# Performance work log

Measured on AMD Instinct MI355X. Metric: run time of the kernel, lower is better.

Reference implementation:

```python
import jax, jax.numpy as jnp
import numpy as np
import math

N_ATOMS = 128
BATCH = 8
FEAT = 64
K_BASIS = 16
N_IRR = 9            # (max_degree+1)^2 with max_degree=2
CUTOFF = 5.0
N_ELEM = 119
SQ3 = 1.7320508075688772

# degree of each of the 9 irrep components: l = 0,1,1,1,2,2,2,2,2
DEG = np.array([0, 1, 1, 1, 2, 2, 2, 2, 2])
_BINOM = jnp.asarray([math.comb(K_BASIS - 1, k) for k in range(K_BASIS)], dtype=jnp.float32)
_KPOW = jnp.arange(K_BASIS, dtype=jnp.float32)


def _sph(u):
    # real spherical harmonics up to l=2 of unit vectors u: [E,3] -> [E,9]
    ux, uy, uz = u[:, 0], u[:, 1], u[:, 2]
    return jnp.stack([
        jnp.ones_like(ux),
        ux, uy, uz,
        SQ3 * ux * uy, SQ3 * uy * uz, 0.5 * (3.0 * uz * uz - 1.0),
        SQ3 * ux * uz, 0.5 * SQ3 * (ux * ux - uy * uy),
    ], axis=-1)


def _basis(disp):
    # disp: [E,3] -> basis [E, 9, K]: Y_lm(u) * reciprocal-Bernstein radial * smooth cutoff
    r = jnp.sqrt(jnp.sum(disp * disp, axis=-1) + 1e-12)      # [E]
    Y = _sph(disp / r[:, None])                              # [E,9]
    w = 1.0 / (1.0 + r)                                      # reciprocal mapping to (0,1]
    rad = _BINOM * w[:, None] ** _KPOW * (1.0 - w)[:, None] ** (K_BASIS - 1.0 - _KPOW)  # [E,K]
    t = (r / CUTOFF) ** 2
    cut = jnp.where(t < 1.0, jnp.exp(1.0 - 1.0 / jnp.maximum(1.0 - t, 1e-12)), 0.0)     # [E]
    return Y[:, :, None] * (rad * cut[:, None])[:, None, :]


def _energy_single(z, pos, embed, WA, WB, W1, b1, W2, W1s, b1s, W2s, w_out, element_bias, dst, src):
    n = pos.shape[0]
    disp = pos[src] - pos[dst]                               # [E,3]
    B = _basis(disp)                                         # [E,9,K]
    # embed atomic numbers into the scalar (l=0) channel
    x = jnp.zeros((n, N_IRR, FEAT), pos.dtype).at[:, 0, :].set(embed[z])
    for i in range(2):  # full-degree message-passing iterations
        xs = x[src]                                          # gather  [E,9,F]
        # equivariant product paths: (scalar src) x (tensor basis) and (tensor src) x (scalar basis)
        mA = jnp.einsum('elk,kf,ef->elf', B, WA[i], xs[:, 0, :])
        mB = xs * jnp.einsum('ek,kf->ef', B[:, 0, :], WB[i])[:, None, :]
        y = jax.ops.segment_sum(mA + mB, dst, num_segments=n)  # scatter-add [N,9,F]
        y = x + y
        y = jnp.einsum('nlf,lfg->nlg', y, W1[i][DEG]).at[:, 0, :].add(b1[i])  # per-degree Dense
        s = y[:, 0, :]
        y = jnp.concatenate([jax.nn.silu(s)[:, None, :],
                             y[:, 1:, :] * jax.nn.sigmoid(s)[:, None, :]], axis=1)  # gated silu
        y = jnp.einsum('nlf,lfg->nlg', y, W2[i][DEG])
        x = x + y
    # last iteration: degree-0 output only (invariant contraction of all degrees)
    xs = x[src]
    mA = jnp.einsum('ek,kf,ef->ef', B[:, 0, :], WA[2], xs[:, 0, :])
    mB = jnp.einsum('elk,elf,kf->ef', B, xs, WB[2])
    y = jax.ops.segment_sum(mA + mB, dst, num_segments=n)    # [N,F]
    x0 = x[:, 0, :]
    h = x0 + y
    h = jax.nn.silu(h @ W1s + b1s) @ W2s
    x0 = x0 + h
    atomic_energies = x0 @ w_out + element_bias[z]           # [N]
    return jnp.sum(atomic_energies)


def setup_inputs() -> dict:
    ks = jax.random.split(jax.random.key(0), 16)
    ii, jj = np.meshgrid(np.arange(N_ATOMS), np.arange(N_ATOMS), indexing='ij')
    mask = ii != jj
    s = 1.0 / np.sqrt(FEAT)
    return {
        'features': jax.random.randint(ks[0], (BATCH, N_ATOMS), 1, N_ELEM, dtype=jnp.int32),
        'positions': jax.random.uniform(ks[1], (BATCH, N_ATOMS, 3), jnp.float32) * 12.0,
        'embed': 0.5 * jax.random.normal(ks[2], (N_ELEM, FEAT), jnp.float32),
        'WA': 0.1 * jax.random.normal(ks[3], (3, K_BASIS, FEAT), jnp.float32),
        'WB': 0.1 * jax.random.normal(ks[4], (3, K_BASIS, FEAT), jnp.float32),
        'W1': s * jax.random.normal(ks[5], (2, 3, FEAT, FEAT), jnp.float32),
        'b1': jnp.zeros((2, FEAT), jnp.float32),
        'W2': 0.1 * s * jax.random.normal(ks[6], (2, 3, FEAT, FEAT), jnp.float32),
        'W1s': s * jax.random.normal(ks[7], (FEAT, FEAT), jnp.float32),
        'b1s': jnp.zeros((FEAT,), jnp.float32),
        'W2s': 0.1 * s * jax.random.normal(ks[8], (FEAT, FEAT), jnp.float32),
        'w_out': 0.1 * jax.random.normal(ks[9], (FEAT,), jnp.float32),
        'element_bias': 0.01 * jax.random.normal(ks[10], (N_ELEM,), jnp.float32),
        'dst_idx': jnp.asarray(ii[mask], jnp.int32),
        'src_idx': jnp.asarray(jj[mask], jnp.int32),
    }


def reference(features, positions, embed, WA, WB, W1, b1, W2, W1s, b1s, W2s, w_out, element_bias, dst_idx, src_idx):
    params = (embed, WA, WB, W1, b1, W2, W1s, b1s, W2s, w_out, element_bias)

    def per_sample(z, pos):
        E, g = jax.value_and_grad(
            lambda p: _energy_single(z, p, *params, dst_idx, src_idx))(pos)
        return E, -g  # energy, forces = -dE/dpos

    return jax.vmap(per_sample)(features, positions)
```

## Files before the change

kernel.cpp:

```cpp
#include <hip/hip_runtime.h>
#include <math.h>

namespace {

constexpr int F   = 64;
constexpr int NA  = 128;
constexpr int NB  = 8;
constexpr int EPN = NA*(NA-1);
constexpr int K   = 16;
constexpr int L   = 9;
constexpr int BE  = NB*EPN;
constexpr int NNLF= NB*NA*L*F;
constexpr int BNF = NB*NA*F;
constexpr int GSP = 8;
constexpr int NSUB= 16;
constexpr float SQ3 = 1.7320508075688772f;

typedef float v2f __attribute__((ext_vector_type(2)));

__device__ __constant__ float BINOM[16] = {1.f,15.f,105.f,455.f,1365.f,3003.f,5005.f,6435.f,
                                           6435.f,5005.f,3003.f,1365.f,455.f,105.f,15.f,1.f};
__device__ __constant__ int DEGC[9] = {0,1,1,1,2,2,2,2,2};

__device__ inline float wred(float v){
  #pragma unroll
  for (int o=32;o>0;o>>=1) v += __shfl_xor(v, o, 64);
  return v;
}

__device__ inline float qreduce(float v0, float v1, float v2, float v3, int lane){
  float a = ((lane&1)? v1 : v0) + __shfl_xor(((lane&1)? v0 : v1), 1, 64);
  float b = ((lane&1)? v3 : v2) + __shfl_xor(((lane&1)? v2 : v3), 1, 64);
  float r = ((lane&2)? b : a) + __shfl_xor(((lane&2)? a : b), 2, 64);
  r += __shfl_xor(r, 4, 64);
  r += __shfl_xor(r, 8, 64);
  r += __shfl_xor(r,16, 64);
  r += __shfl_xor(r,32, 64);
  return r;
}

__global__ void k_prep(const float* W1, const float* W2, const float* W1s,
                       const float* W2s, const float* wout,
                       float* W1T, float* W2T, float* W1sT, float* dsp,
                       float* outbuf){
  int idx = blockIdx.x*256 + threadIdx.x;
  if (idx < 6*F*F){
    int rem = idx % (F*F); int m = idx/(F*F); int g = rem/F, f = rem%F;
    W1T[idx] = W1[(m*F+f)*F+g];
    W2T[idx] = W2[(m*F+f)*F+g];
  } else if (idx < 6*F*F + F*F){
    int rem = idx - 6*F*F; int g = rem/F, f = rem%F;
    W1sT[rem] = W1s[f*F+g];
  } else if (idx < 6*F*F + F*F + F){
    int f = idx - 6*F*F - F*F;
    float s=0.f;
    for (int g=0; g<F; g++) s += W2s[f*F+g]*wout[g];
    dsp[f]=s;
  } else if (idx < 6*F*F + F*F + F + NB + NB*NA*3){
    outbuf[idx - (6*F*F + F*F + F)] = 0.f;
  }
}

__global__ void k_geom(const float* __restrict__ pos, const int* __restrict__ dsti,
                       const int* __restrict__ srci,
                       float* __restrict__ U, float* __restrict__ Rr,
                       float* __restrict__ Rp){
  int idx = blockIdx.x*256 + threadIdx.x;
  if (idx >= BE) return;
  int b = idx / EPN, e = idx % EPN;
  int d = dsti[e], s = srci[e];
  const float* pb = pos + (size_t)b*NA*3;
  float dx = pb[s*3+0]-pb[d*3+0];
  float dy = pb[s*3+1]-pb[d*3+1];
  float dz = pb[s*3+2]-pb[d*3+2];
  float ss = dx*dx+dy*dy+dz*dz + 1e-12f;
  float r  = sqrtf(ss);
  float ir = 1.f/r;
  U[(size_t)idx*4+0]=dx*ir; U[(size_t)idx*4+1]=dy*ir;
  U[(size_t)idx*4+2]=dz*ir; U[(size_t)idx*4+3]=ir;
  float w = 1.f/(1.f+r), v = 1.f - w;
  float wp[16], vp[16];
  wp[0]=1.f; vp[0]=1.f;
  #pragma unroll
  for (int k=1;k<16;k++){ wp[k]=wp[k-1]*w; vp[k]=vp[k-1]*v; }
  float t = (r*0.2f)*(r*0.2f);
  float cut=0.f, dcut=0.f;
  if (t < 1.f){
    float e1 = 1.f - t;
    float m  = fmaxf(e1, 1e-12f);
    cut = expf(1.f - 1.f/m);
    if (e1 > 1e-12f) dcut = -cut/(e1*e1) * (2.f*r*0.04f);
  }
  float nww = -w*w;
  #pragma unroll
  for (int k=0;k<16;k++){
    float rad = BINOM[k]*wp[k]*vp[15-k];
    float t1 = (k>0)  ? (float)k      * wp[k-1]*vp[15-k] : 0.f;
    float t2 = (k<15) ? (float)(15-k) * wp[k]  *vp[14-k] : 0.f;
    float dradr = BINOM[k]*(t1-t2)*nww;
    Rr[(size_t)idx*16+k] = rad*cut;
    Rp[(size_t)idx*16+k] = dradr*cut + rad*dcut;
  }
}

__global__ void k_init_x(const int* __restrict__ z, const float* __restrict__ embed,
                         float* __restrict__ x0){
  int b = blockIdx.x / NA, n = blockIdx.x % NA, f = threadIdx.x;
  int zi = z[b*NA+n];
  float* row = x0 + ((size_t)(b*NA+n))*L*F;
  row[f] = embed[(size_t)zi*F+f];
  #pragma unroll
  for (int l=1;l<L;l++) row[l*F+f]=0.f;
}

template<bool FIRST>
__global__ __launch_bounds__(64,6) void k_edge_fwd(const float* __restrict__ x,
    const float* __restrict__ WA, const float* __restrict__ WB,
    const float* __restrict__ U, const float* __restrict__ Rr,
    float* __restrict__ aggP){
  int bid = blockIdx.x;
  int g = bid & (GSP-1), bn = bid >> 3;
  int b = bn >> 7, n = bn & (NA-1);
  int f = threadIdx.x;
  v2f wab[K];
  #pragma unroll
  for (int k=0;k<K;k++){ v2f t = {WA[k*F+f], WB[k*F+f]}; wab[k]=t; }
  float acc[L];
  #pragma unroll
  for (int l=0;l<L;l++) acc[l]=0.f;
  const float* xb = x + (size_t)b*NA*L*F;
  int c0 = g*NSUB, c1 = min(c0+NSUB, NA-1);
  #pragma unroll 2
  for (int c=c0; c<c1; ++c){
    int e = n*(NA-1)+c;
    int j = c + (c>=n);
    size_t ge = (size_t)b*EPN + e;
    const float* Re = Rr + ge*K;
    v2f AB = {0.f, 0.f};
    #pragma unroll
    for (int k=0;k<K;k++) AB += Re[k]*wab[k];
    float RA=AB.x, RB=AB.y;
    float ux=U[ge*4+0], uy=U[ge*4+1], uz=U[ge*4+2];
    float Y4=SQ3*ux*uy, Y5=SQ3*uy*uz, Y6=0.5f*(3.f*uz*uz-1.f);
    float Y7=SQ3*ux*uz, Y8=0.5f*SQ3*(ux*ux-uy*uy);
    const float* xr = xb + (size_t)j*L*F + f;
    float xs0 = xr[0];
    float t1 = RA*xs0;
    acc[0] += t1 + xs0*RB;
    if (FIRST){
      acc[1] += ux*t1; acc[2] += uy*t1; acc[3] += uz*t1;
      acc[4] += Y4*t1; acc[5] += Y5*t1; acc[6] += Y6*t1;
      acc[7] += Y7*t1; acc[8] += Y8*t1;
    } else {
      acc[1] += ux*t1 + xr[1*F]*RB;
      acc[2] += uy*t1 + xr[2*F]*RB;
      acc[3] += uz*t1 + xr[3*F]*RB;
      acc[4] += Y4*t1 + xr[4*F]*RB;
      acc[5] += Y5*t1 + xr[5*F]*RB;
      acc[6] += Y6*t1 + xr[6*F]*RB;
      acc[7] += Y7*t1 + xr[7*F]*RB;
      acc[8] += Y8*t1 + xr[8*F]*RB;
    }
  }
  float* ar = aggP + (size_t)g*NNLF + (size_t)bn*L*F + f;
  #pragma unroll
  for (int l=0;l<L;l++) ar[l*F] = acc[l];
}

__global__ __launch_bounds__(256) void k_node_fwd(const float* __restrict__ x,
    const float* __restrict__ aggP, const float* __restrict__ W1,
    const float* __restrict__ b1, const float* __restrict__ W2,
    float* __restrict__ y2out, float* __restrict__ xout){
  __shared__ float sh[L*F];
  __shared__ float yb[L*F];
  __shared__ float zb[L*F];
  int t = threadIdx.x, g = t&63, w = t>>6;
  size_t base = ((size_t)blockIdx.x)*L*F;
  for (int idx=t; idx<L*F; idx+=256){
    float s = x[base+idx];
    #pragma unroll
    for (int sl=0; sl<GSP; sl++) s += aggP[(size_t)sl*NNLF + base + idx];
    sh[idx]=s;
  }
  __syncthreads();
  for (int l=w; l<L; l+=4){
    const float* W = W1 + DEGC[l]*F*F + g;
    float s=0.f;
    for (int ff=0; ff<F; ff++) s += sh[l*F+ff]*W[(size_t)ff*F];
    if (l==0) s += b1[g];
    y2out[base+l*F+g]=s;
    yb[l*F+g]=s;
  }
  __syncthreads();
  float sv = yb[g];
  float sg = 1.f/(1.f+expf(-sv));
  for (int l=w; l<L; l+=4)
    zb[l*F+g] = (l==0)? sv*sg : yb[l*F+g]*sg;
  __syncthreads();
  for (int l=w; l<L; l+=4){
    const float* W = W2 + DEGC[l]*F*F + g;
    float s=0.f;
    for (int ff=0; ff<F; ff++) s += zb[l*F+ff]*W[(size_t)ff*F];
    xout[base+l*F+g] = x[base+l*F+g] + s;
  }
}

__global__ __launch_bounds__(64,6) void k_redge_fwd(const float* __restrict__ x2,
    const float* __restrict__ WA2, const float* __restrict__ WB2,
    const float* __restrict__ U, const float* __restrict__ Rr,
    float* __restrict__ yRp){
  int bid = blockIdx.x;
  int g = bid & (GSP-1), bn = bid >> 3;
  int b = bn >> 7, n = bn & (NA-1);
  int f = threadIdx.x;
  v2f wab[K];
  #pragma unroll
  for (int k=0;k<K;k++){ v2f t = {WA2[k*F+f], WB2[k*F+f]}; wab[k]=t; }
  float acc=0.f;
  const float* xb = x2 + (size_t)b*NA*L*F;
  int c0 = g*NSUB, c1 = min(c0+NSUB, NA-1);
  #pragma unroll 2
  for (int c=c0; c<c1; ++c){
    int e = n*(NA-1)+c;
    int j = c + (c>=n);
    size_t ge = (size_t)b*EPN + e;
    const float* Re = Rr + ge*K;
    v2f AB = {0.f, 0.f};
    #pragma unroll
    for (int k=0;k<K;k++) AB += Re[k]*wab[k];
    float RA=AB.x, RB=AB.y;
    float ux=U[ge*4+0], uy=U[ge*4+1], uz=U[ge*4+2];
    const float* xr = xb + (size_t)j*L*F + f;
    float xs0 = xr[0];
    float T = xs0
            + ux*xr[1*F] + uy*xr[2*F] + uz*xr[3*F]
            + (SQ3*ux*uy)*xr[4*F] + (SQ3*uy*uz)*xr[5*F]
            + (0.5f*(3.f*uz*uz-1.f))*xr[6*F]
            + (SQ3*ux*uz)*xr[7*F] + (0.5f*SQ3*(ux*ux-uy*uy))*xr[8*F];
    acc += RA*xs0 + RB*T;
  }
  yRp[(size_t)g*BNF + (size_t)bn*F + f] = acc;
}

__global__ __launch_bounds__(256) void k_rnode_fwd(const int* __restrict__ z,
    const float* __restrict__ x2, const float* __restrict__ yRp,
    const float* __restrict__ W1s, const float* __restrict__ b1s,
    const float* __restrict__ W2s, const float* __restrict__ wout,
    const float* __restrict__ ebias, float* __restrict__ pW, float* Eout){
  __shared__ float sh[F];
  __shared__ float part[4][F];
  int t = threadIdx.x, g = t&63, w = t>>6;
  int bnn = blockIdx.x;
  int b = bnn >> 7;
  size_t base = (size_t)bnn*L*F;
  size_t nb   = (size_t)bnn*F;
  if (t < F){
    float s = x2[base+t];
    #pragma unroll
    for (int sl=0; sl<GSP; sl++) s += yRp[(size_t)sl*BNF + nb + t];
    sh[t]=s;
  }
  __syncthreads();
  float pp=0.f;
  for (int ff=w*16; ff<w*16+16; ff++) pp += sh[ff]*W1s[(size_t)ff*F+g];
  part[w][g]=pp;
  __syncthreads();
  float p = part[0][g]+part[1][g]+part[2][g]+part[3][g] + b1s[g];
  if (w==0) pW[nb+g]=p;
  float sp = p/(1.f+expf(-p));
  __syncthreads();
  if (w==0) sh[g]=sp;
  __syncthreads();
  float h=0.f;
  for (int ff=w*16; ff<w*16+16; ff++) h += sh[ff]*W2s[(size_t)ff*F+g];
  part[w][g]=h;
  __syncthreads();
  if (w==0){
    float h2 = part[0][g]+part[1][g]+part[2][g]+part[3][g];
    float x0v = x2[base+g];
    float en = wred((x0v+h2)*wout[g]);
    if (g==0) atomicAdd(Eout+b, en + ebias[z[bnn]]);
  }
}

__global__ __launch_bounds__(256) void k_rnode_bwd(const float* __restrict__ pW,
    const float* __restrict__ dsp, const float* __restrict__ W1sT,
    const float* __restrict__ wout, float* __restrict__ dyR, float* __restrict__ dxA){
  __shared__ float sh[F];
  __shared__ float part[4][F];
  int t = threadIdx.x, g = t&63, w = t>>6;
  size_t nb = (size_t)blockIdx.x*F;
  size_t base = (size_t)blockIdx.x*L*F;
  if (t < F){
    float p  = pW[nb+t];
    float sgm = 1.f/(1.f+expf(-p));
    sh[t] = dsp[t]*sgm*(1.f + p*(1.f-sgm));
  }
  __syncthreads();
  float s=0.f;
  for (int ff=w*16; ff<w*16+16; ff++) s += sh[ff]*W1sT[(size_t)ff*F+g];
  part[w][g]=s;
  __syncthreads();
  if (w==0){
    float dh1 = part[0][g]+part[1][g]+part[2][g]+part[3][g];
    dyR[nb+g]=dh1;
    dxA[base+g] = wout[g]+dh1;
  }
  for (int idx=t; idx<(L-1)*F; idx+=256) dxA[base+F+idx]=0.f;
}

__global__ __launch_bounds__(64,6) void k_redge_bwd(const float* __restrict__ x2,
    const float* __restrict__ WA2, const float* __restrict__ WB2,
    const float* __restrict__ U, const float* __restrict__ Rr,
    const float* __restrict__ Rp, const float* __restrict__ dyR,
    float* __restrict__ partP, float* Fout){
  int bid = blockIdx.x;
  int g = bid & (GSP-1), bn = bid >> 3;
  int b = bn >> 7, j = bn & (NA-1);
  int f = threadIdx.x, m = f & 3;
  v2f wab[K];
  #pragma unroll
  for (int k=0;k<K;k++){ v2f t = {WA2[k*F+f], WB2[k*F+f]}; wab[k]=t; }
  size_t xbase = ((size_t)bn)*L*F;
  float xs[L];
  #pragma unroll
  for (int l=0;l<L;l++) xs[l]=x2[xbase+l*F+f];
  float acc[L];
  #pragma unroll
  for (int l=0;l<L;l++) acc[l]=0.f;
  float sdd=0.f;
  int i0 = g*NSUB, i1 = min(i0+NSUB, NA-1);
  #pragma unroll 2
  for (int ii=i0; ii<i1; ++ii){
    int i = ii + (ii>=j);
    int c = (j<i)? j : j-1;
    size_t ge = (size_t)b*EPN + i*(NA-1)+c;
    float gv = dyR[(size_t)(b*NA+i)*F+f];
    const float* Re = Rr + ge*K;
    const float* Pe = Rp + ge*K;
    v2f RAB = {0.f,0.f}, PAB = {0.f,0.f};
    #pragma unroll
    for (int k=0;k<K;k++){ RAB += Re[k]*wab[k]; PAB += Pe[k]*wab[k]; }
    float RA=RAB.x, RB=RAB.y, PA=PAB.x, PB=PAB.y;
    float ux=U[ge*4+0], uy=U[ge*4+1], uz=U[ge*4+2], ir=U[ge*4+3];
    float Y4=SQ3*ux*uy, Y5=SQ3*uy*uz, Y6=0.5f*(3.f*uz*uz-1.f);
    float Y7=SQ3*ux*uz, Y8=0.5f*SQ3*(ux*ux-uy*uy);
    float T = xs[0] + ux*xs[1]+uy*xs[2]+uz*xs[3]
            + Y4*xs[4]+Y5*xs[5]+Y6*xs[6]+Y7*xs[7]+Y8*xs[8];
    float X0 = xs[1] + SQ3*(uy*xs[4]+uz*xs[7]+ux*xs[8]);
    float X1 = xs[2] + SQ3*(ux*xs[4]+uz*xs[5]-uy*xs[8]);
    float X2 = xs[3] + SQ3*(uy*xs[5]+ux*xs[7]) + 3.f*uz*xs[6];
    acc[0] += gv*(RA+RB);
    acc[1] += gv*ux*RB; acc[2] += gv*uy*RB; acc[3] += gv*uz*RB;
    acc[4] += gv*Y4*RB; acc[5] += gv*Y5*RB; acc[6] += gv*Y6*RB;
    acc[7] += gv*Y7*RB; acc[8] += gv*Y8*RB;
    float gRB = gv*RB;
    float r4 = qreduce(gRB*X0, gRB*X1, gRB*X2, gv*(xs[0]*PA + T*PB), f);
    float um = (m==0)?ux : (m==1)?uy : (m==2)?uz : 0.f;
    float q = r4*um;
    q += __shfl_xor(q,1,64); q += __shfl_xor(q,2,64);
    float SR = __shfl(r4, f|3, 64);
    float dd = (r4 - q*um)*ir + SR*um;
    if (f<3) atomicAdd(&Fout[(size_t)(b*NA+i)*3+f], dd);
    sdd += dd;
  }
  float* ar = partP + (size_t)g*NNLF + xbase + f;
  #pragma unroll
  for (int l=0;l<L;l++) ar[l*F] = acc[l];
  if (f<3) atomicAdd(&Fout[(size_t)(b*NA+j)*3+f], -sdd);
}

template<bool WDX>
__global__ __launch_bounds__(256) void k_node_bwd(const float* __restrict__ dxIn,
    const float* __restrict__ partP, const float* __restrict__ y2W,
    const float* __restrict__ W1T, const float* __restrict__ W2T,
    float* __restrict__ dagg, float* __restrict__ dxOut){
  __shared__ float A[L*F];
  __shared__ float D3[L*F];
  __shared__ float Bb[L*F];
  __shared__ float prt[4][F];
  int t = threadIdx.x, g = t&63, w = t>>6;
  size_t base = ((size_t)blockIdx.x)*L*F;
  for (int idx=t; idx<L*F; idx+=256){
    float s = dxIn[base+idx];
    #pragma unroll
    for (int sl=0; sl<GSP; sl++) s += partP[(size_t)sl*NNLF + base + idx];
    A[idx]=s;
  }
  __syncthreads();
  float pc=0.f;
  for (int l=w; l<L; l+=4){
    const float* W = W2T + DEGC[l]*F*F + g;
    float s=0.f;
    for (int ff=0; ff<F; ff++) s += A[l*F+ff]*W[(size_t)ff*F];
    D3[l*F+g]=s;
    if (l>0) pc += s * y2W[base+l*F+g];
  }
  prt[w][g]=pc;
  __syncthreads();
  float sv = y2W[base+g];
  float sg = 1.f/(1.f+expf(-sv));
  for (int l=w; l<L; l+=4){
    float v;
    if (l==0){
      float sum = prt[0][g]+prt[1][g]+prt[2][g]+prt[3][g];
      v = D3[g]*sg*(1.f+sv*(1.f-sg)) + sum*sg*(1.f-sg);
    } else {
      v = D3[l*F+g]*sg;
    }
    Bb[l*F+g]=v;
  }
  __syncthreads();
  for (int l=w; l<L; l+=4){
    const float* W = W1T + DEGC[l]*F*F + g;
    float s=0.f;
    for (int ff=0; ff<F; ff++) s += Bb[l*F+ff]*W[(size_t)ff*F];
    dagg[base+l*F+g]=s;
    if (WDX) dxOut[base+l*F+g] = A[l*F+g] + s;
  }
}

template<bool WDX, bool FIRST>
__global__ __launch_bounds__(64,6) void k_edge_bwd(const float* __restrict__ xI,
    const float* __restrict__ WA, const float* __restrict__ WB,
    const float* __restrict__ U, const float* __restrict__ Rr,
    const float* __restrict__ Rp, const float* __restrict__ dagg,
    float* __restrict__ partP, float* Fout){
  int bid = blockIdx.x;
  int g = bid & (GSP-1), bn = bid >> 3;
  int b = bn >> 7, j = bn & (NA-1);
  int f = threadIdx.x, m = f & 3;
  v2f wab[K];
  #pragma unroll
  for (int k=0;k<K;k++){ v2f t = {WA[k*F+f], WB[k*F+f]}; wab[k]=t; }
  size_t xbase = ((size_t)bn)*L*F;
  float xs[L];
  xs[0] = xI[xbase+f];
  #pragma unroll
  for (int l=1;l<L;l++) xs[l] = FIRST ? 0.f : xI[xbase+l*F+f];
  float acc[L]; float acc0=0.f;
  #pragma unroll
  for (int l=0;l<L;l++) acc[l]=0.f;
  float sdd=0.f;
  int i0 = g*NSUB, i1 = min(i0+NSUB, NA-1);
  #pragma unroll 2
  for (int ii=i0; ii<i1; ++ii){
    int i = ii + (ii>=j);
    int c = (j<i)? j : j-1;
    size_t ge = (size_t)b*EPN + i*(NA-1)+c;
    const float* gr = dagg + ((size_t)(b*NA+i))*L*F + f;
    float gl[L];
    #pragma unroll
    for (int l=0;l<L;l++) gl[l]=gr[l*F];
    const float* Re = Rr + ge*K;
    const float* Pe = Rp + ge*K;
    v2f RAB = {0.f,0.f}, PAB = {0.f,0.f};
    #pragma unroll
    for (int k=0;k<K;k++){ RAB += Re[k]*wab[k]; PAB += Pe[k]*wab[k]; }
    float RA=RAB.x, RB=RAB.y, PA=PAB.x, PB=PAB.y;
    float ux=U[ge*4+0], uy=U[ge*4+1], uz=U[ge*4+2], ir=U[ge*4+3];
    float Y4=SQ3*ux*uy, Y5=SQ3*uy*uz, Y6=0.5f*(3.f*uz*uz-1.f);
    float Y7=SQ3*ux*uz, Y8=0.5f*SQ3*(ux*ux-uy*uy);
    float gy = gl[0] + gl[1]*ux+gl[2]*uy+gl[3]*uz
             + gl[4]*Y4+gl[5]*Y5+gl[6]*Y6+gl[7]*Y7+gl[8]*Y8;
    float gx;
    if (FIRST){
      gx = gl[0]*xs[0];
    } else {
      gx = 0.f;
      #pragma unroll
      for (int l=0;l<L;l++) gx += gl[l]*xs[l];
    }
    float G0 = gl[1] + SQ3*(uy*gl[4]+uz*gl[7]+ux*gl[8]);
    float G1 = gl[2] + SQ3*(ux*gl[4]+uz*gl[5]-uy*gl[8]);
    float G2 = gl[3] + SQ3*(uy*gl[5]+ux*gl[7]) + 3.f*uz*gl[6];
    if (WDX){
      acc0 += gy*RA;
      #pragma unroll
      for (int l=0;l<L;l++) acc[l] += gl[l]*RB;
    }
    float cm = RA*xs[0];
    float r4 = qreduce(cm*G0, cm*G1, cm*G2, gy*xs[0]*PA + gx*PB, f);
    float um = (m==0)?ux : (m==1)?uy : (m==2)?uz : 0.f;
    float q = r4*um;
    q += __shfl_xor(q,1,64); q += __shfl_xor(q,2,64);
    float SR = __shfl(r4, f|3, 64);
    float dd = (r4 - q*um)*ir + SR*um;
    if (f<3) atomicAdd(&Fout[(size_t)(b*NA+i)*3+f], dd);
    sdd += dd;
  }
  if (WDX){
    float* ar = partP + (size_t)g*NNLF + xbase + f;
    ar[0] = acc0 + acc[0];
    #pragma unroll
    for (int l=1;l<L;l++) ar[l*F] = acc[l];
  }
  if (f<3) atomicAdd(&Fout[(size_t)(b*NA+j)*3+f], -sdd);
}

}

extern "C" void kernel_launch(void* const* d_in, const int* in_sizes, int n_in,
                              void* d_out, int out_size, void* d_ws, size_t ws_size,
                              hipStream_t stream){
  (void)in_sizes; (void)n_in; (void)out_size; (void)ws_size;
  const int*   z     = (const int*)  d_in[0];
  const float* pos   = (const float*)d_in[1];
  const float* emb   = (const float*)d_in[2];
  const float* WA    = (const float*)d_in[3];
  const float* WB    = (const float*)d_in[4];
  const float* W1    = (const float*)d_in[5];
  const float* b1    = (const float*)d_in[6];
  const float* W2    = (const float*)d_in[7];
  const float* W1s   = (const float*)d_in[8];
  const float* b1s   = (const float*)d_in[9];
  const float* W2s   = (const float*)d_in[10];
  const float* wout  = (const float*)d_in[11];
  const float* ebias = (const float*)d_in[12];
  const int*   dsti  = (const int*)  d_in[13];
  const int*   srci  = (const int*)  d_in[14];

  float* w    = (float*)d_ws;
  float* U    = w;
  float* Rr   = U    + (size_t)BE*4;
  float* Rp   = Rr   + (size_t)BE*16;
  float* x0   = Rp   + (size_t)BE*16;
  float* x1   = x0   + NNLF;
  float* x2   = x1   + NNLF;
  float* y2b  = x2   + NNLF;
  float* part = y2b  + 2*(size_t)NNLF;
  float* yRp  = part + (size_t)GSP*NNLF;
  float* pW   = yRp  + (size_t)GSP*BNF;
  float* dyR  = pW   + BNF;
  float* dxA  = dyR  + BNF;
  float* dxO  = dxA  + NNLF;
  float* dagg = dxO  + NNLF;
  float* W1T  = dagg + NNLF;
  float* W2T  = W1T  + 6*F*F;
  float* W1sT = W2T  + 6*F*F;
  float* dspv = W1sT + F*F;

  float* Eout = (float*)d_out;
  float* Fout = Eout + NB;

  dim3 bn(NB*NA);
  dim3 be(NB*NA*GSP);

  k_prep  <<<126, 256, 0, stream>>>(W1, W2, W1s, W2s, wout, W1T, W2T, W1sT, dspv, Eout);
  k_geom  <<<(BE+255)/256, 256, 0, stream>>>(pos, dsti, srci, U, Rr, Rp);
  k_init_x<<<bn, 64, 0, stream>>>(z, emb, x0);

  k_edge_fwd<true ><<<be, 64, 0, stream>>>(x0, WA,     WB,     U, Rr, part);
  k_node_fwd<<<bn, 256, 0, stream>>>(x0, part, W1,       b1,   W2,       y2b,      x1);
  k_edge_fwd<false><<<be, 64, 0, stream>>>(x1, WA+K*F, WB+K*F, U, Rr, part);
  k_node_fwd<<<bn, 256, 0, stream>>>(x1, part, W1+3*F*F, b1+F, W2+3*F*F, y2b+NNLF, x2);
  k_redge_fwd<<<be, 64, 0, stream>>>(x2, WA+2*K*F, WB+2*K*F, U, Rr, yRp);
  k_rnode_fwd<<<bn, 256, 0, stream>>>(z, x2, yRp, W1s, b1s, W2s, wout, ebias, pW, Eout);

  k_rnode_bwd<<<bn, 256, 0, stream>>>(pW, dspv, W1sT, wout, dyR, dxA);
  k_redge_bwd<<<be, 64, 0, stream>>>(x2, WA+2*K*F, WB+2*K*F, U, Rr, Rp, dyR, part, Fout);
  k_node_bwd<true ><<<bn, 256, 0, stream>>>(dxA, part, y2b+NNLF, W1T+3*F*F, W2T+3*F*F, dagg, dxO);
  k_edge_bwd<true ,false><<<be, 64, 0, stream>>>(x1, WA+K*F, WB+K*F, U, Rr, Rp, dagg, part, Fout);
  k_node_bwd<false><<<bn, 256, 0, stream>>>(dxO, part, y2b, W1T, W2T, dagg, nullptr);
  k_edge_bwd<false,true ><<<be, 64, 0, stream>>>(x0, WA, WB, U, Rr, Rp, dagg, nullptr, Fout);
}
```

Before: 421.7 us.

## Reduce edge partials in-block via shared memory instead of global partial buffers

Edge kernels now launch one 512-thread block per node, with eight wavefronts each covering a slice of neighbours. Their partial sums are reduced in LDS and written once (or added into dxA/dxO), so node kernels no longer read eight global partial slabs. Per-node force atomics are also collapsed to one per block, and the tangential projection in the force term is folded algebraically so one shuffle reduction disappears. Larger blocks with a __syncthreads may limit occupancy compared with the many small 64-thread blocks used before.

```diff
diff --git a/kernel.cpp b/kernel.cpp
--- a/kernel.cpp
+++ b/kernel.cpp
@@ -12,7 +12,7 @@
 constexpr int BE  = NB*EPN;
 constexpr int NNLF= NB*NA*L*F;
 constexpr int BNF = NB*NA*F;
-constexpr int GSP = 8;
+constexpr int WPB = 8;
 constexpr int NSUB= 16;
 constexpr float SQ3 = 1.7320508075688772f;
 
@@ -114,22 +114,22 @@
 }
 
 template<bool FIRST>
-__global__ __launch_bounds__(64,6) void k_edge_fwd(const float* __restrict__ x,
+__global__ __launch_bounds__(512,8) void k_edge_fwd(const float* __restrict__ x,
     const float* __restrict__ WA, const float* __restrict__ WB,
     const float* __restrict__ U, const float* __restrict__ Rr,
-    float* __restrict__ aggP){
-  int bid = blockIdx.x;
-  int g = bid & (GSP-1), bn = bid >> 3;
+    float* __restrict__ agg){
+  __shared__ float sh[WPB][L*F];
+  int bn = blockIdx.x;
   int b = bn >> 7, n = bn & (NA-1);
-  int f = threadIdx.x;
+  int t = threadIdx.x, f = t&63, wv = t>>6;
   v2f wab[K];
   #pragma unroll
-  for (int k=0;k<K;k++){ v2f t = {WA[k*F+f], WB[k*F+f]}; wab[k]=t; }
+  for (int k=0;k<K;k++){ v2f tt = {WA[k*F+f], WB[k*F+f]}; wab[k]=tt; }
   float acc[L];
   #pragma unroll
   for (int l=0;l<L;l++) acc[l]=0.f;
   const float* xb = x + (size_t)b*NA*L*F;
-  int c0 = g*NSUB, c1 = min(c0+NSUB, NA-1);
+  int c0 = wv*NSUB, c1 = min(c0+NSUB, NA-1);
   #pragma unroll 2
   for (int c=c0; c<c1; ++c){
     int e = n*(NA-1)+c;
@@ -162,13 +162,20 @@
       acc[8] += Y8*t1 + xr[8*F]*RB;
     }
   }
-  float* ar = aggP + (size_t)g*NNLF + (size_t)bn*L*F + f;
-  #pragma unroll
-  for (int l=0;l<L;l++) ar[l*F] = acc[l];
+  #pragma unroll
+  for (int l=0;l<L;l++) sh[wv][l*F+f] = acc[l];
+  __syncthreads();
+  float* ar = agg + (size_t)bn*L*F;
+  for (int idx=t; idx<L*F; idx+=512){
+    float s = sh[0][idx];
+    #pragma unroll
+    for (int w8=1; w8<WPB; w8++) s += sh[w8][idx];
+    ar[idx] = s;
+  }
 }
 
 __global__ __launch_bounds__(256) void k_node_fwd(const float* __restrict__ x,
-    const float* __restrict__ aggP, const float* __restrict__ W1,
+    const float* __restrict__ agg, const float* __restrict__ W1,
     const float* __restrict__ b1, const float* __restrict__ W2,
     float* __restrict__ y2out, float* __restrict__ xout){
   __shared__ float sh[L*F];
@@ -176,12 +183,8 @@
   __shared__ float zb[L*F];
   int t = threadIdx.x, g = t&63, w = t>>6;
   size_t base = ((size_t)blockIdx.x)*L*F;
-  for (int idx=t; idx<L*F; idx+=256){
-    float s = x[base+idx];
-    #pragma unroll
-    for (int sl=0; sl<GSP; sl++) s += aggP[(size_t)sl*NNLF + base + idx];
-    sh[idx]=s;
-  }
+  for (int idx=t; idx<L*F; idx+=256)
+    sh[idx] = x[base+idx] + agg[base+idx];
   __syncthreads();
   for (int l=w; l<L; l+=4){
     const float* W = W1 + DEGC[l]*F*F + g;
@@ -205,20 +208,20 @@
   }
 }
 
-__global__ __launch_bounds__(64,6) void k_redge_fwd(const float* __restrict__ x2,
+__global__ __launch_bounds__(512,8) void k_redge_fwd(const float* __restrict__ x2,
     const float* __restrict__ WA2, const float* __restrict__ WB2,
     const float* __restrict__ U, const float* __restrict__ Rr,
-    float* __restrict__ yRp){
-  int bid = blockIdx.x;
-  int g = bid & (GSP-1), bn = bid >> 3;
+    float* __restrict__ yR){
+  __shared__ float sh[WPB][F];
+  int bn = blockIdx.x;
   int b = bn >> 7, n = bn & (NA-1);
-  int f = threadIdx.x;
+  int t = threadIdx.x, f = t&63, wv = t>>6;
   v2f wab[K];
   #pragma unroll
-  for (int k=0;k<K;k++){ v2f t = {WA2[k*F+f], WB2[k*F+f]}; wab[k]=t; }
+  for (int k=0;k<K;k++){ v2f tt = {WA2[k*F+f], WB2[k*F+f]}; wab[k]=tt; }
   float acc=0.f;
   const float* xb = x2 + (size_t)b*NA*L*F;
-  int c0 = g*NSUB, c1 = min(c0+NSUB, NA-1);
+  int c0 = wv*NSUB, c1 = min(c0+NSUB, NA-1);
   #pragma unroll 2
   for (int c=c0; c<c1; ++c){
     int e = n*(NA-1)+c;
@@ -239,11 +242,18 @@
             + (SQ3*ux*uz)*xr[7*F] + (0.5f*SQ3*(ux*ux-uy*uy))*xr[8*F];
     acc += RA*xs0 + RB*T;
   }
-  yRp[(size_t)g*BNF + (size_t)bn*F + f] = acc;
+  sh[wv][f]=acc;
+  __syncthreads();
+  if (t < F){
+    float s = sh[0][t];
+    #pragma unroll
+    for (int w8=1; w8<WPB; w8++) s += sh[w8][t];
+    yR[(size_t)bn*F + t] = s;
+  }
 }
 
 __global__ __launch_bounds__(256) void k_rnode_fwd(const int* __restrict__ z,
-    const float* __restrict__ x2, const float* __restrict__ yRp,
+    const float* __restrict__ x2, const float* __restrict__ yR,
     const float* __restrict__ W1s, const float* __restrict__ b1s,
     const float* __restrict__ W2s, const float* __restrict__ wout,
     const float* __restrict__ ebias, float* __restrict__ pW, float* Eout){
@@ -254,12 +264,7 @@
   int b = bnn >> 7;
   size_t base = (size_t)bnn*L*F;
   size_t nb   = (size_t)bnn*F;
-  if (t < F){
-    float s = x2[base+t];
-    #pragma unroll
-    for (int sl=0; sl<GSP; sl++) s += yRp[(size_t)sl*BNF + nb + t];
-    sh[t]=s;
-  }
+  if (t < F) sh[t] = x2[base+t] + yR[nb+t];
   __syncthreads();
   float pp=0.f;
   for (int ff=w*16; ff<w*16+16; ff++) pp += sh[ff]*W1s[(size_t)ff*F+g];
@@ -309,18 +314,19 @@
   for (int idx=t; idx<(L-1)*F; idx+=256) dxA[base+F+idx]=0.f;
 }
 
-__global__ __launch_bounds__(64,6) void k_redge_bwd(const float* __restrict__ x2,
+__global__ __launch_bounds__(512,8) void k_redge_bwd(const float* __restrict__ x2,
     const float* __restrict__ WA2, const float* __restrict__ WB2,
     const float* __restrict__ U, const float* __restrict__ Rr,
     const float* __restrict__ Rp, const float* __restrict__ dyR,
-    float* __restrict__ partP, float* Fout){
-  int bid = blockIdx.x;
-  int g = bid & (GSP-1), bn = bid >> 3;
+    float* __restrict__ dxA, float* Fout){
+  __shared__ float sh[WPB][L*F];
+  __shared__ float shS[WPB][4];
+  int bn = blockIdx.x;
   int b = bn >> 7, j = bn & (NA-1);
-  int f = threadIdx.x, m = f & 3;
+  int t = threadIdx.x, f = t&63, wv = t>>6, m = f&3;
   v2f wab[K];
   #pragma unroll
-  for (int k=0;k<K;k++){ v2f t = {WA2[k*F+f], WB2[k*F+f]}; wab[k]=t; }
+  for (int k=0;k<K;k++){ v2f tt = {WA2[k*F+f], WB2[k*F+f]}; wab[k]=tt; }
   size_t xbase = ((size_t)bn)*L*F;
   float xs[L];
   #pragma unroll
@@ -329,7 +335,7 @@
   #pragma unroll
   for (int l=0;l<L;l++) acc[l]=0.f;
   float sdd=0.f;
-  int i0 = g*NSUB, i1 = min(i0+NSUB, NA-1);
+  int i0 = wv*NSUB, i1 = min(i0+NSUB, NA-1);
   #pragma unroll 2
   for (int ii=i0; ii<i1; ++ii){
     int i = ii + (ii>=j);
@@ -355,24 +361,37 @@
     acc[4] += gv*Y4*RB; acc[5] += gv*Y5*RB; acc[6] += gv*Y6*RB;
     acc[7] += gv*Y7*RB; acc[8] += gv*Y8*RB;
     float gRB = gv*RB;
-    float r4 = qreduce(gRB*X0, gRB*X1, gRB*X2, gv*(xs[0]*PA + T*PB), f);
+    float dotX = ux*X0 + uy*X1 + uz*X2;
+    float v3 = gv*(xs[0]*PA + T*PB) - gRB*dotX*ir;
+    float r4 = qreduce(gRB*X0, gRB*X1, gRB*X2, v3, f);
+    float SR = __shfl(r4, f|3, 64);
     float um = (m==0)?ux : (m==1)?uy : (m==2)?uz : 0.f;
-    float q = r4*um;
-    q += __shfl_xor(q,1,64); q += __shfl_xor(q,2,64);
-    float SR = __shfl(r4, f|3, 64);
-    float dd = (r4 - q*um)*ir + SR*um;
+    float dd = r4*ir + SR*um;
     if (f<3) atomicAdd(&Fout[(size_t)(b*NA+i)*3+f], dd);
     sdd += dd;
   }
-  float* ar = partP + (size_t)g*NNLF + xbase + f;
-  #pragma unroll
-  for (int l=0;l<L;l++) ar[l*F] = acc[l];
-  if (f<3) atomicAdd(&Fout[(size_t)(b*NA+j)*3+f], -sdd);
+  #pragma unroll
+  for (int l=0;l<L;l++) sh[wv][l*F+f]=acc[l];
+  if (f<3) shS[wv][f]=sdd;
+  __syncthreads();
+  float* ar = dxA + xbase;
+  for (int idx=t; idx<L*F; idx+=512){
+    float s = sh[0][idx];
+    #pragma unroll
+    for (int w8=1; w8<WPB; w8++) s += sh[w8][idx];
+    ar[idx] += s;
+  }
+  if (t<3){
+    float s = shS[0][t];
+    #pragma unroll
+    for (int w8=1; w8<WPB; w8++) s += shS[w8][t];
+    atomicAdd(&Fout[(size_t)bn*3+t], -s);
+  }
 }
 
 template<bool WDX>
 __global__ __launch_bounds__(256) void k_node_bwd(const float* __restrict__ dxIn,
-    const float* __restrict__ partP, const float* __restrict__ y2W,
+    const float* __restrict__ y2W,
     const float* __restrict__ W1T, const float* __restrict__ W2T,
     float* __restrict__ dagg, float* __restrict__ dxOut){
   __shared__ float A[L*F];
@@ -381,12 +400,7 @@
   __shared__ float prt[4][F];
   int t = threadIdx.x, g = t&63, w = t>>6;
   size_t base = ((size_t)blockIdx.x)*L*F;
-  for (int idx=t; idx<L*F; idx+=256){
-    float s = dxIn[base+idx];
-    #pragma unroll
-    for (int sl=0; sl<GSP; sl++) s += partP[(size_t)sl*NNLF + base + idx];
-    A[idx]=s;
-  }
+  for (int idx=t; idx<L*F; idx+=256) A[idx]=dxIn[base+idx];
   __syncthreads();
   float pc=0.f;
   for (int l=w; l<L; l+=4){
@@ -421,18 +435,19 @@
 }
 
 template<bool WDX, bool FIRST>
-__global__ __launch_bounds__(64,6) void k_edge_bwd(const float* __restrict__ xI,
+__global__ __launch_bounds__(512,8) void k_edge_bwd(const float* __restrict__ xI,
     const float* __restrict__ WA, const float* __restrict__ WB,
     const float* __restrict__ U, const float* __restrict__ Rr,
     const float* __restrict__ Rp, const float* __restrict__ dagg,
-    float* __restrict__ partP, float* Fout){
-  int bid = blockIdx.x;
-  int g = bid & (GSP-1), bn = bid >> 3;
+    float* __restrict__ dxOut, float* Fout){
+  __shared__ float sh[WPB][L*F];
+  __shared__ float shS[WPB][4];
+  int bn = blockIdx.x;
   int b = bn >> 7, j = bn & (NA-1);
-  int f = threadIdx.x, m = f & 3;
+  int t = threadIdx.x, f = t&63, wv = t>>6, m = f&3;
   v2f wab[K];
   #pragma unroll
-  for (int k=0;k<K;k++){ v2f t = {WA[k*F+f], WB[k*F+f]}; wab[k]=t; }
+  for (int k=0;k<K;k++){ v2f tt = {WA[k*F+f], WB[k*F+f]}; wab[k]=tt; }
   size_t xbase = ((size_t)bn)*L*F;
   float xs[L];
   xs[0] = xI[xbase+f];
@@ -442,7 +457,7 @@
   #pragma unroll
   for (int l=0;l<L;l++) acc[l]=0.f;
   float sdd=0.f;
-  int i0 = g*NSUB, i1 = min(i0+NSUB, NA-1);
+  int i0 = wv*NSUB, i1 = min(i0+NSUB, NA-1);
   #pragma unroll 2
   for (int ii=i0; ii<i1; ++ii){
     int i = ii + (ii>=j);
@@ -480,22 +495,37 @@
       for (int l=0;l<L;l++) acc[l] += gl[l]*RB;
     }
     float cm = RA*xs[0];
-    float r4 = qreduce(cm*G0, cm*G1, cm*G2, gy*xs[0]*PA + gx*PB, f);
+    float dotG = ux*G0 + uy*G1 + uz*G2;
+    float v3 = gy*xs[0]*PA + gx*PB - cm*dotG*ir;
+    float r4 = qreduce(cm*G0, cm*G1, cm*G2, v3, f);
+    float SR = __shfl(r4, f|3, 64);
     float um = (m==0)?ux : (m==1)?uy : (m==2)?uz : 0.f;
-    float q = r4*um;
-    q += __shfl_xor(q,1,64); q += __shfl_xor(q,2,64);
-    float SR = __shfl(r4, f|3, 64);
-    float dd = (r4 - q*um)*ir + SR*um;
+    float dd = r4*ir + SR*um;
     if (f<3) atomicAdd(&Fout[(size_t)(b*NA+i)*3+f], dd);
     sdd += dd;
   }
   if (WDX){
-    float* ar = partP + (size_t)g*NNLF + xbase + f;
-    ar[0] = acc0 + acc[0];
-    #pragma unroll
-    for (int l=1;l<L;l++) ar[l*F] = acc[l];
-  }
-  if (f<3) atomicAdd(&Fout[(size_t)(b*NA+j)*3+f], -sdd);
+    sh[wv][f] = acc0 + acc[0];
+    #pragma unroll
+    for (int l=1;l<L;l++) sh[wv][l*F+f] = acc[l];
+  }
+  if (f<3) shS[wv][f]=sdd;
+  __syncthreads();
+  if (WDX){
+    float* ar = dxOut + xbase;
+    for (int idx=t; idx<L*F; idx+=512){
+      float s = sh[0][idx];
+      #pragma unroll
+      for (int w8=1; w8<WPB; w8++) s += sh[w8][idx];
+      ar[idx] += s;
+    }
+  }
+  if (t<3){
+    float s = shS[0][t];
+    #pragma unroll
+    for (int w8=1; w8<WPB; w8++) s += shS[w8][t];
+    atomicAdd(&Fout[(size_t)bn*3+t], -s);
+  }
 }
 
 }
@@ -528,9 +558,9 @@
   float* x1   = x0   + NNLF;
   float* x2   = x1   + NNLF;
   float* y2b  = x2   + NNLF;
-  float* part = y2b  + 2*(size_t)NNLF;
-  float* yRp  = part + (size_t)GSP*NNLF;
-  float* pW   = yRp  + (size_t)GSP*BNF;
+  float* agg  = y2b  + 2*(size_t)NNLF;
+  float* yR   = agg  + NNLF;
+  float* pW   = yR   + BNF;
   float* dyR  = pW   + BNF;
   float* dxA  = dyR  + BNF;
   float* dxO  = dxA  + NNLF;
@@ -544,23 +574,22 @@
   float* Fout = Eout + NB;
 
   dim3 bn(NB*NA);
-  dim3 be(NB*NA*GSP);
 
   k_prep  <<<126, 256, 0, stream>>>(W1, W2, W1s, W2s, wout, W1T, W2T, W1sT, dspv, Eout);
   k_geom  <<<(BE+255)/256, 256, 0, stream>>>(pos, dsti, srci, U, Rr, Rp);
   k_init_x<<<bn, 64, 0, stream>>>(z, emb, x0);
 
-  k_edge_fwd<true ><<<be, 64, 0, stream>>>(x0, WA,     WB,     U, Rr, part);
-  k_node_fwd<<<bn, 256, 0, stream>>>(x0, part, W1,       b1,   W2,       y2b,      x1);
-  k_edge_fwd<false><<<be, 64, 0, stream>>>(x1, WA+K*F, WB+K*F, U, Rr, part);
-  k_node_fwd<<<bn, 256, 0, stream>>>(x1, part, W1+3*F*F, b1+F, W2+3*F*F, y2b+NNLF, x2);
-  k_redge_fwd<<<be, 64, 0, stream>>>(x2, WA+2*K*F, WB+2*K*F, U, Rr, yRp);
-  k_rnode_fwd<<<bn, 256, 0, stream>>>(z, x2, yRp, W1s, b1s, W2s, wout, ebias, pW, Eout);
+  k_edge_fwd<true ><<<bn, 512, 0, stream>>>(x0, WA,     WB,     U, Rr, agg);
+  k_node_fwd<<<bn, 256, 0, stream>>>(x0, agg, W1,       b1,   W2,       y2b,      x1);
+  k_edge_fwd<false><<<bn, 512, 0, stream>>>(x1, WA+K*F, WB+K*F, U, Rr, agg);
+  k_node_fwd<<<bn, 256, 0, stream>>>(x1, agg, W1+3*F*F, b1+F, W2+3*F*F, y2b+NNLF, x2);
+  k_redge_fwd<<<bn, 512, 0, stream>>>(x2, WA+2*K*F, WB+2*K*F, U, Rr, yR);
+  k_rnode_fwd<<<bn, 256, 0, stream>>>(z, x2, yR, W1s, b1s, W2s, wout, ebias, pW, Eout);
 
   k_rnode_bwd<<<bn, 256, 0, stream>>>(pW, dspv, W1sT, wout, dyR, dxA);
-  k_redge_bwd<<<be, 64, 0, stream>>>(x2, WA+2*K*F, WB+2*K*F, U, Rr, Rp, dyR, part, Fout);
-  k_node_bwd<true ><<<bn, 256, 0, stream>>>(dxA, part, y2b+NNLF, W1T+3*F*F, W2T+3*F*F, dagg, dxO);
-  k_edge_bwd<true ,false><<<be, 64, 0, stream>>>(x1, WA+K*F, WB+K*F, U, Rr, Rp, dagg, part, Fout);
-  k_node_bwd<false><<<bn, 256, 0, stream>>>(dxO, part, y2b, W1T, W2T, dagg, nullptr);
-  k_edge_bwd<false,true ><<<be, 64, 0, stream>>>(x0, WA, WB, U, Rr, Rp, dagg, nullptr, Fout);
-}
+  k_redge_bwd<<<bn, 512, 0, stream>>>(x2, WA+2*K*F, WB+2*K*F, U, Rr, Rp, dyR, dxA, Fout);
+  k_node_bwd<true ><<<bn, 256, 0, stream>>>(dxA, y2b+NNLF, W1T+3*F*F, W2T+3*F*F, dagg, dxO);
+  k_edge_bwd<true ,false><<<bn, 512, 0, stream>>>(x1, WA+K*F, WB+K*F, U, Rr, Rp, dagg, dxO, Fout);
+  k_node_bwd<false><<<bn, 256, 0, stream>>>(dxO, y2b, W1T, W2T, dagg, nullptr);
+  k_edge_bwd<false,true ><<<bn, 512, 0, stream>>>(x0, WA, WB, U, Rr, Rp, dagg, nullptr, Fout);
+}
```

After: 1.042 ms. 147% more time.

## Halve edge-kernel grid split, fold force projection into the reduction, drop packed math

Applied to the files above, without the earlier changes.

The per-node edge range is now split into 4 sub-blocks of 32 edges instead of 8 of 16, and launch bounds drop from 6 to 4 waves. That means fewer partial-sum buffers and weight reloads, but also less parallelism in flight. The packed v2f multiply-adds become scalar dual accumulators, and the unroll-2 pragma is removed from the backward loops. In the backward kernels the radial projection term is folded algebraically into the fourth qreduce lane, which removes two shuffles and a multiply per edge.

```diff
diff --git a/kernel.cpp b/kernel.cpp
--- a/kernel.cpp
+++ b/kernel.cpp
@@ -12,11 +12,9 @@
 constexpr int BE  = NB*EPN;
 constexpr int NNLF= NB*NA*L*F;
 constexpr int BNF = NB*NA*F;
-constexpr int GSP = 8;
-constexpr int NSUB= 16;
+constexpr int GSP = 4;
+constexpr int NSUB= 32;
 constexpr float SQ3 = 1.7320508075688772f;
-
-typedef float v2f __attribute__((ext_vector_type(2)));
 
 __device__ __constant__ float BINOM[16] = {1.f,15.f,105.f,455.f,1365.f,3003.f,5005.f,6435.f,
                                            6435.f,5005.f,3003.f,1365.f,455.f,105.f,15.f,1.f};
@@ -114,17 +112,17 @@
 }
 
 template<bool FIRST>
-__global__ __launch_bounds__(64,6) void k_edge_fwd(const float* __restrict__ x,
+__global__ __launch_bounds__(64,4) void k_edge_fwd(const float* __restrict__ x,
     const float* __restrict__ WA, const float* __restrict__ WB,
     const float* __restrict__ U, const float* __restrict__ Rr,
     float* __restrict__ aggP){
   int bid = blockIdx.x;
-  int g = bid & (GSP-1), bn = bid >> 3;
+  int g = bid & (GSP-1), bn = bid >> 2;
   int b = bn >> 7, n = bn & (NA-1);
   int f = threadIdx.x;
-  v2f wab[K];
-  #pragma unroll
-  for (int k=0;k<K;k++){ v2f t = {WA[k*F+f], WB[k*F+f]}; wab[k]=t; }
+  float wa[K], wb[K];
+  #pragma unroll
+  for (int k=0;k<K;k++){ wa[k]=WA[k*F+f]; wb[k]=WB[k*F+f]; }
   float acc[L];
   #pragma unroll
   for (int l=0;l<L;l++) acc[l]=0.f;
@@ -136,10 +134,9 @@
     int j = c + (c>=n);
     size_t ge = (size_t)b*EPN + e;
     const float* Re = Rr + ge*K;
-    v2f AB = {0.f, 0.f};
-    #pragma unroll
-    for (int k=0;k<K;k++) AB += Re[k]*wab[k];
-    float RA=AB.x, RB=AB.y;
+    float RA=0.f, RB=0.f;
+    #pragma unroll
+    for (int k=0;k<K;k++){ float rk=Re[k]; RA += rk*wa[k]; RB += rk*wb[k]; }
     float ux=U[ge*4+0], uy=U[ge*4+1], uz=U[ge*4+2];
     float Y4=SQ3*ux*uy, Y5=SQ3*uy*uz, Y6=0.5f*(3.f*uz*uz-1.f);
     float Y7=SQ3*ux*uz, Y8=0.5f*SQ3*(ux*ux-uy*uy);
@@ -205,17 +202,17 @@
   }
 }
 
-__global__ __launch_bounds__(64,6) void k_redge_fwd(const float* __restrict__ x2,
+__global__ __launch_bounds__(64,4) void k_redge_fwd(const float* __restrict__ x2,
     const float* __restrict__ WA2, const float* __restrict__ WB2,
     const float* __restrict__ U, const float* __restrict__ Rr,
     float* __restrict__ yRp){
   int bid = blockIdx.x;
-  int g = bid & (GSP-1), bn = bid >> 3;
+  int g = bid & (GSP-1), bn = bid >> 2;
   int b = bn >> 7, n = bn & (NA-1);
   int f = threadIdx.x;
-  v2f wab[K];
-  #pragma unroll
-  for (int k=0;k<K;k++){ v2f t = {WA2[k*F+f], WB2[k*F+f]}; wab[k]=t; }
+  float wa[K], wb[K];
+  #pragma unroll
+  for (int k=0;k<K;k++){ wa[k]=WA2[k*F+f]; wb[k]=WB2[k*F+f]; }
   float acc=0.f;
   const float* xb = x2 + (size_t)b*NA*L*F;
   int c0 = g*NSUB, c1 = min(c0+NSUB, NA-1);
@@ -225,10 +222,9 @@
     int j = c + (c>=n);
     size_t ge = (size_t)b*EPN + e;
     const float* Re = Rr + ge*K;
-    v2f AB = {0.f, 0.f};
-    #pragma unroll
-    for (int k=0;k<K;k++) AB += Re[k]*wab[k];
-    float RA=AB.x, RB=AB.y;
+    float RA=0.f, RB=0.f;
+    #pragma unroll
+    for (int k=0;k<K;k++){ float rk=Re[k]; RA += rk*wa[k]; RB += rk*wb[k]; }
     float ux=U[ge*4+0], uy=U[ge*4+1], uz=U[ge*4+2];
     const float* xr = xb + (size_t)j*L*F + f;
     float xs0 = xr[0];
@@ -309,18 +305,18 @@
   for (int idx=t; idx<(L-1)*F; idx+=256) dxA[base+F+idx]=0.f;
 }
 
-__global__ __launch_bounds__(64,6) void k_redge_bwd(const float* __restrict__ x2,
+__global__ __launch_bounds__(64,4) void k_redge_bwd(const float* __restrict__ x2,
     const float* __restrict__ WA2, const float* __restrict__ WB2,
     const float* __restrict__ U, const float* __restrict__ Rr,
     const float* __restrict__ Rp, const float* __restrict__ dyR,
     float* __restrict__ partP, float* Fout){
   int bid = blockIdx.x;
-  int g = bid & (GSP-1), bn = bid >> 3;
+  int g = bid & (GSP-1), bn = bid >> 2;
   int b = bn >> 7, j = bn & (NA-1);
   int f = threadIdx.x, m = f & 3;
-  v2f wab[K];
-  #pragma unroll
-  for (int k=0;k<K;k++){ v2f t = {WA2[k*F+f], WB2[k*F+f]}; wab[k]=t; }
+  float wa[K], wb[K];
+  #pragma unroll
+  for (int k=0;k<K;k++){ wa[k]=WA2[k*F+f]; wb[k]=WB2[k*F+f]; }
   size_t xbase = ((size_t)bn)*L*F;
   float xs[L];
   #pragma unroll
@@ -330,7 +326,6 @@
   for (int l=0;l<L;l++) acc[l]=0.f;
   float sdd=0.f;
   int i0 = g*NSUB, i1 = min(i0+NSUB, NA-1);
-  #pragma unroll 2
   for (int ii=i0; ii<i1; ++ii){
     int i = ii + (ii>=j);
     int c = (j<i)? j : j-1;
@@ -338,10 +333,10 @@
     float gv = dyR[(size_t)(b*NA+i)*F+f];
     const float* Re = Rr + ge*K;
     const float* Pe = Rp + ge*K;
-    v2f RAB = {0.f,0.f}, PAB = {0.f,0.f};
-    #pragma unroll
-    for (int k=0;k<K;k++){ RAB += Re[k]*wab[k]; PAB += Pe[k]*wab[k]; }
-    float RA=RAB.x, RB=RAB.y, PA=PAB.x, PB=PAB.y;
+    float RA=0.f,RB=0.f,PA=0.f,PB=0.f;
+    #pragma unroll
+    for (int k=0;k<K;k++){ float rk=Re[k],pk=Pe[k];
+      RA+=rk*wa[k]; RB+=rk*wb[k]; PA+=pk*wa[k]; PB+=pk*wb[k]; }
     float ux=U[ge*4+0], uy=U[ge*4+1], uz=U[ge*4+2], ir=U[ge*4+3];
     float Y4=SQ3*ux*uy, Y5=SQ3*uy*uz, Y6=0.5f*(3.f*uz*uz-1.f);
     float Y7=SQ3*ux*uz, Y8=0.5f*SQ3*(ux*ux-uy*uy);
@@ -355,19 +350,19 @@
     acc[4] += gv*Y4*RB; acc[5] += gv*Y5*RB; acc[6] += gv*Y6*RB;
     acc[7] += gv*Y7*RB; acc[8] += gv*Y8*RB;
     float gRB = gv*RB;
-    float r4 = qreduce(gRB*X0, gRB*X1, gRB*X2, gv*(xs[0]*PA + T*PB), f);
+    float dotX = ux*X0 + uy*X1 + uz*X2;
+    float v3 = gv*(xs[0]*PA + T*PB) - gRB*dotX*ir;
+    float r4 = qreduce(gRB*X0, gRB*X1, gRB*X2, v3, f);
+    float SR = __shfl(r4, f|3, 64);
     float um = (m==0)?ux : (m==1)?uy : (m==2)?uz : 0.f;
-    float q = r4*um;
-    q += __shfl_xor(q,1,64); q += __shfl_xor(q,2,64);
-    float SR = __shfl(r4, f|3, 64);
-    float dd = (r4 - q*um)*ir + SR*um;
+    float dd = r4*ir + SR*um;
     if (f<3) atomicAdd(&Fout[(size_t)(b*NA+i)*3+f], dd);
     sdd += dd;
   }
   float* ar = partP + (size_t)g*NNLF + xbase + f;
   #pragma unroll
   for (int l=0;l<L;l++) ar[l*F] = acc[l];
-  if (f<3) atomicAdd(&Fout[(size_t)(b*NA+j)*3+f], -sdd);
+  if (f<3) atomicAdd(&Fout[(size_t)bn*3+f], -sdd);
 }
 
 template<bool WDX>
@@ -421,18 +416,18 @@
 }
 
 template<bool WDX, bool FIRST>
-__global__ __launch_bounds__(64,6) void k_edge_bwd(const float* __restrict__ xI,
+__global__ __launch_bounds__(64,4) void k_edge_bwd(const float* __restrict__ xI,
     const float* __restrict__ WA, const float* __restrict__ WB,
     const float* __restrict__ U, const float* __restrict__ Rr,
     const float* __restrict__ Rp, const float* __restrict__ dagg,
     float* __restrict__ partP, float* Fout){
   int bid = blockIdx.x;
-  int g = bid & (GSP-1), bn = bid >> 3;
+  int g = bid & (GSP-1), bn = bid >> 2;
   int b = bn >> 7, j = bn & (NA-1);
   int f = threadIdx.x, m = f & 3;
-  v2f wab[K];
-  #pragma unroll
-  for (int k=0;k<K;k++){ v2f t = {WA[k*F+f], WB[k*F+f]}; wab[k]=t; }
+  float wa[K], wb[K];
+  #pragma unroll
+  for (int k=0;k<K;k++){ wa[k]=WA[k*F+f]; wb[k]=WB[k*F+f]; }
   size_t xbase = ((size_t)bn)*L*F;
   float xs[L];
   xs[0] = xI[xbase+f];
@@ -443,7 +438,6 @@
   for (int l=0;l<L;l++) acc[l]=0.f;
   float sdd=0.f;
   int i0 = g*NSUB, i1 = min(i0+NSUB, NA-1);
-  #pragma unroll 2
   for (int ii=i0; ii<i1; ++ii){
     int i = ii + (ii>=j);
     int c = (j<i)? j : j-1;
@@ -454,10 +448,10 @@
     for (int l=0;l<L;l++) gl[l]=gr[l*F];
     const float* Re = Rr + ge*K;
     const float* Pe = Rp + ge*K;
-    v2f RAB = {0.f,0.f}, PAB = {0.f,0.f};
-    #pragma unroll
-    for (int k=0;k<K;k++){ RAB += Re[k]*wab[k]; PAB += Pe[k]*wab[k]; }
-    float RA=RAB.x, RB=RAB.y, PA=PAB.x, PB=PAB.y;
+    float RA=0.f,RB=0.f,PA=0.f,PB=0.f;
+    #pragma unroll
+    for (int k=0;k<K;k++){ float rk=Re[k],pk=Pe[k];
+      RA+=rk*wa[k]; RB+=rk*wb[k]; PA+=pk*wa[k]; PB+=pk*wb[k]; }
     float ux=U[ge*4+0], uy=U[ge*4+1], uz=U[ge*4+2], ir=U[ge*4+3];
     float Y4=SQ3*ux*uy, Y5=SQ3*uy*uz, Y6=0.5f*(3.f*uz*uz-1.f);
     float Y7=SQ3*ux*uz, Y8=0.5f*SQ3*(ux*ux-uy*uy);
@@ -480,12 +474,12 @@
       for (int l=0;l<L;l++) acc[l] += gl[l]*RB;
     }
     float cm = RA*xs[0];
-    float r4 = qreduce(cm*G0, cm*G1, cm*G2, gy*xs[0]*PA + gx*PB, f);
+    float dotG = ux*G0 + uy*G1 + uz*G2;
+    float v3 = gy*xs[0]*PA + gx*PB - cm*dotG*ir;
+    float r4 = qreduce(cm*G0, cm*G1, cm*G2, v3, f);
+    float SR = __shfl(r4, f|3, 64);
     float um = (m==0)?ux : (m==1)?uy : (m==2)?uz : 0.f;
-    float q = r4*um;
-    q += __shfl_xor(q,1,64); q += __shfl_xor(q,2,64);
-    float SR = __shfl(r4, f|3, 64);
-    float dd = (r4 - q*um)*ir + SR*um;
+    float dd = r4*ir + SR*um;
     if (f<3) atomicAdd(&Fout[(size_t)(b*NA+i)*3+f], dd);
     sdd += dd;
   }
@@ -495,7 +489,7 @@
     #pragma unroll
     for (int l=1;l<L;l++) ar[l*F] = acc[l];
   }
-  if (f<3) atomicAdd(&Fout[(size_t)(b*NA+j)*3+f], -sdd);
+  if (f<3) atomicAdd(&Fout[(size_t)bn*3+f], -sdd);
 }
 
 }
```

Result: faster. 399.5 us (-5.3%).
